# Optimization experiments

Measured on AMD Instinct MI355X. Metric: run time of the kernel, lower is better.

The kernel has to match this reference:

```python
import jax, jax.numpy as jnp
import numpy as np

B, T, M, D = 8, 512, 16, 128
P, H = 256, 8
E = P // H


def setup_inputs() -> dict:
    key = jax.random.key(0)
    ks = jax.random.split(key, 5)
    inp = jax.random.normal(ks[0], (B, T, M, D), dtype=jnp.float32)
    mask = jax.random.randint(ks[1], (B, T, M), 0, 2).astype(bool)
    sc = 1.0 / np.sqrt(D).astype(np.float32)
    Wq = jax.random.normal(ks[2], (D, P), dtype=jnp.float32) * sc
    Wk = jax.random.normal(ks[3], (D, P), dtype=jnp.float32) * sc
    Wv = jax.random.normal(ks[4], (D, P), dtype=jnp.float32) * sc
    z = jnp.zeros((P,), dtype=jnp.float32)
    return {"inp": inp, "mask": mask, "Wq": Wq, "bq": z, "Wk": Wk, "bk": z, "Wv": Wv, "bv": z}


def _split_heads(x):
    # (b, t, m, h*e) -> (b, m, h, t, e)
    b, t, m, _ = x.shape
    return x.reshape(b, t, m, H, E).transpose(0, 2, 3, 1, 4)


def reference(inp, mask, Wq, bq, Wk, bk, Wv, bv):
    q = _split_heads(inp @ Wq + bq)
    k = _split_heads(inp @ Wk + bk)
    v = _split_heads(inp @ Wv + bv)
    # scores over time axis per (batch, modality, head): (b, m, h, t, t)
    score = jnp.einsum('bmhte,bmhse->bmhts', q, k) / np.float32(np.sqrt(E))
    kmask = mask.transpose(0, 2, 1)[:, :, None, None, :]  # (b, m, 1, 1, t)
    score = jnp.where(kmask, score, -jnp.inf)
    weight = jax.nn.softmax(score, axis=-1)
    weight = jnp.where(kmask, weight, jnp.zeros((), weight.dtype))
    out = jnp.einsum('bmhts,bmhse->bmhte', weight, v)
    b, m, h, t, e = out.shape
    return out.transpose(0, 3, 1, 2, 4).reshape(b, t, m, h * e)
```

## Files before the change

### kernel.cpp

```cpp
#include <hip/hip_runtime.h>
#include <stdint.h>

#define B_ 8
#define T_ 512
#define M_ 16
#define D_ 128
#define P_ 256
#define H_ 8
#define E_ 32

typedef __attribute__((ext_vector_type(8))) short  short8;
typedef __attribute__((ext_vector_type(4))) short  short4v;
typedef __attribute__((ext_vector_type(4))) float  float4v;
typedef __attribute__((ext_vector_type(2))) unsigned int uint2v;
typedef __attribute__((ext_vector_type(4))) unsigned int uint4v;
typedef __attribute__((ext_vector_type(2))) __bf16 bf16x2;

#define MFMA32(a,b,c) __builtin_amdgcn_mfma_f32_16x16x32_bf16(a,b,c,0,0,0)
#define EXP2F(x) __builtin_amdgcn_exp2f(x)

#define C2 0.2550332772062413f

static __device__ __forceinline__ unsigned short f2bf(float x){
  unsigned int u = __builtin_bit_cast(unsigned int, x);
  u += 0x7FFFu + ((u >> 16) & 1u);
  return (unsigned short)(u >> 16);
}

static __device__ __forceinline__ unsigned int pk2(float a, float b){
  bf16x2 h; h[0] = (__bf16)a; h[1] = (__bf16)b;
  return __builtin_bit_cast(unsigned int, h);
}

static __device__ __forceinline__ short4v pack4(float4v v){
  uint2v u; u.x = pk2(v[0], v[1]); u.y = pk2(v[2], v[3]);
  return __builtin_bit_cast(short4v, u);
}

static __device__ __forceinline__ short8 pack8(float4v a, float4v b){
  uint4v u; u.x = pk2(a[0],a[1]); u.y = pk2(a[2],a[3]);
  u.z = pk2(b[0],b[1]); u.w = pk2(b[2],b[3]);
  return __builtin_bit_cast(short8, u);
}

static __device__ __forceinline__ short8 cat44(short4v lo, short4v hi){
  short8 r;
  r[0]=lo[0]; r[1]=lo[1]; r[2]=lo[2]; r[3]=lo[3];
  r[4]=hi[0]; r[5]=hi[1]; r[6]=hi[2]; r[7]=hi[3];
  return r;
}

__global__ void prep(const float* __restrict__ Wq, const float* __restrict__ Wk,
                     const float* __restrict__ Wv, uint16_t* __restrict__ WT){
  int idx = blockIdx.x*256 + threadIdx.x;
  int p = idx & (P_-1);
  int d = (idx >> 8) & (D_-1);
  int z = idx >> 15;
  int col = p;
  if (z < 2){
    int w = p & 31;
    int e = ((w>>2)&3)*8 + ((w>>4)&1)*4 + (w&3);
    col = (p & ~31) | e;
  }
  const float* W = (z==0) ? Wq : (z==1) ? Wk : Wv;
  float sc = (z==0) ? C2 : 1.0f;
  WT[(z<<15) + (p<<7) + d] = f2bf(W[d*P_ + col] * sc);
}

__global__ __launch_bounds__(512, 4) void attn_fused(
    const float* __restrict__ inp, const uint16_t* __restrict__ WT,
    const float* __restrict__ bq, const float* __restrict__ bk,
    const float* __restrict__ bv, const int* __restrict__ mask,
    float* __restrict__ out){
  __shared__ __align__(16) uint16_t smem[(65536 + 2048)/2];
  uint16_t* Kb   = smem;
  uint16_t* Vt   = smem + 16384;
  float*    Mrow = (float*)(smem + 32768);

  const int bx = blockIdx.x;
  const int h = bx >> 7, bm = bx & 127;
  const int b = bm >> 4, m = bm & 15;
  const int tid = threadIdx.x;
  const int wave = tid >> 6, lane = tid & 63;
  const int q4 = lane >> 4, c = lane & 15;
  const int t0 = wave*64;

  {
    int mv = mask[((size_t)(b*T_ + tid))*M_ + m];
    Mrow[tid] = mv ? 0.0f : -1e30f;
  }

  short8 af[4][4];
  {
    const float* src0 = inp + (size_t)((b*T_ + t0)*M_ + m)*D_ + c*4;
    for (int hh=0; hh<2; hh++){
      for (int jb=0; jb<2; jb++){
        float4v stg[8];
        for (int j=0; j<8; j++){
          int r = jb*32 + j*4 + q4;
          stg[j] = *(const float4v*)(src0 + (size_t)r*(M_*D_) + hh*64);
        }
        for (int j=0; j<8; j++){
          int r = t0 + jb*32 + j*4 + q4;
          short4v s4 = pack4(stg[j]);
          *(short4v*)(smem + r*64 + ((((c>>1) ^ (r&7))<<3) + ((c&1)<<2))) = s4;
        }
      }
      for (int tj=0; tj<4; tj++){
        int r2 = t0 + tj*16 + c;
        af[tj][hh*2+0] = *(const short8*)(smem + r2*64 + (((q4    ) ^ (r2&7))<<3));
        af[tj][hh*2+1] = *(const short8*)(smem + r2*64 + (((q4 | 4) ^ (r2&7))<<3));
      }
    }
  }
  __syncthreads();

  const uint16_t* WQ = WT                       + (size_t)(h*E_)*D_;
  const uint16_t* WK = WT + (size_t)1*P_*D_     + (size_t)(h*E_)*D_;
  const uint16_t* WV = WT + (size_t)2*P_*D_     + (size_t)(h*E_)*D_;
  float4v zf = {0.f,0.f,0.f,0.f};

  for (int eh=0; eh<2; eh++){
    float4v ka[4]; for (int j=0;j<4;j++) ka[j]=zf;
    for (int kc=0; kc<4; kc++){
      short8 w = *(const short8*)(WK + (size_t)(eh*16 + c)*D_ + kc*32 + q4*8);
      for (int sj=0; sj<4; sj++) ka[sj] = MFMA32(w, af[sj][kc], ka[sj]);
    }
    float4v bk4 = *(const float4v*)(bk + h*E_ + q4*8 + eh*4);
    for (int sj=0; sj<4; sj++){
      int s = t0 + sj*16 + c;
      short4v kv = pack4(ka[sj] + bk4);
      *(short4v*)(Kb + s*32 + ((q4 ^ (s&3))<<3) + eh*4) = kv;
    }
  }
  for (int eh=0; eh<2; eh++){
    float4v va[4]; for (int j=0;j<4;j++) va[j]=zf;
    for (int kc=0; kc<4; kc++){
      short8 w = *(const short8*)(WV + (size_t)(eh*16 + c)*D_ + kc*32 + q4*8);
      for (int sj=0; sj<4; sj++) va[sj] = MFMA32(w, af[sj][kc], va[sj]);
    }
    float4v bv4 = *(const float4v*)(bv + h*E_ + eh*16 + q4*4);
    for (int sj=0; sj<4; sj++){
      int s = t0 + sj*16 + c;
      short4v vv = pack4(va[sj] + bv4);
      for (int r=0; r<4; r++){
        int e = eh*16 + q4*4 + r;
        Vt[e*T_ + ((((s>>2) + 2*e) & 127)*4) + (s&3)] = (uint16_t)vv[r];
      }
    }
  }
  short8 q8[4];
  {
    short4v qtmp[4][2];
    for (int eh=0; eh<2; eh++){
      float4v qa[4]; for (int j=0;j<4;j++) qa[j]=zf;
      for (int kc=0; kc<4; kc++){
        short8 w = *(const short8*)(WQ + (size_t)(eh*16 + c)*D_ + kc*32 + q4*8);
        for (int tj=0; tj<4; tj++) qa[tj] = MFMA32(w, af[tj][kc], qa[tj]);
      }
      float4v bq4 = *(const float4v*)(bq + h*E_ + q4*8 + eh*4);
      bq4 *= C2;
      for (int tj=0; tj<4; tj++) qtmp[tj][eh] = pack4(qa[tj] + bq4);
    }
    for (int tj=0; tj<4; tj++) q8[tj] = cat44(qtmp[tj][0], qtmp[tj][1]);
  }
  __syncthreads();

  float4v O[4][2], L4[4];
  for (int i=0;i<4;i++){ O[i][0]=zf; O[i][1]=zf; L4[i]=zf; }
  const short one_bf = (short)0x3F80;
  short8 ones8;
  for (int i=0;i<8;i++) ones8[i] = one_bf;

  for (int sb=0; sb<16; sb++){
    const int sq = sb*32;
    float4v mm0 = *(const float4v*)(Mrow + sq + q4*4);
    float4v mm1 = *(const float4v*)(Mrow + sq + 16 + q4*4);
    const int srow0 = sq + c, srow1 = sq + 16 + c;
    short8 kb8_0 = *(const short8*)(Kb + srow0*32 + ((q4 ^ (srow0&3))<<3));
    short8 kb8_1 = *(const short8*)(Kb + srow1*32 + ((q4 ^ (srow1&3))<<3));
    const int u0 = sb*8 + q4, u1 = u0 + 4;
    short4v vA0 = *(const short4v*)(Vt + (size_t)c*T_      + ((u0 + 2*c     ) & 127)*4);
    short4v vA1 = *(const short4v*)(Vt + (size_t)c*T_      + ((u1 + 2*c     ) & 127)*4);
    short4v vB0 = *(const short4v*)(Vt + (size_t)(16+c)*T_ + ((u0 + 32 + 2*c) & 127)*4);
    short4v vB1 = *(const short4v*)(Vt + (size_t)(16+c)*T_ + ((u1 + 32 + 2*c) & 127)*4);
    short8 V8_0 = cat44(vA0, vA1);
    short8 V8_1 = cat44(vB0, vB1);
    __builtin_amdgcn_s_setprio(1);
    for (int tj=0; tj<4; tj++){
      float4v st0 = MFMA32(kb8_0, q8[tj], mm0);
      float4v st1 = MFMA32(kb8_1, q8[tj], mm1);
      float4v p0, p1;
      p0[0] = EXP2F(st0[0]); p0[1] = EXP2F(st0[1]);
      p0[2] = EXP2F(st0[2]); p0[3] = EXP2F(st0[3]);
      p1[0] = EXP2F(st1[0]); p1[1] = EXP2F(st1[1]);
      p1[2] = EXP2F(st1[2]); p1[3] = EXP2F(st1[3]);
      short8 A8 = pack8(p0, p1);
      O[tj][0] = MFMA32(A8, V8_0, O[tj][0]);
      O[tj][1] = MFMA32(A8, V8_1, O[tj][1]);
      L4[tj]   = MFMA32(A8, ones8, L4[tj]);
    }
    __builtin_amdgcn_s_setprio(0);
  }

  for (int ti=0; ti<4; ti++){
    float4v linv;
    for (int r=0; r<4; r++) linv[r] = __builtin_amdgcn_rcpf(L4[ti][r]);
    for (int ej=0; ej<2; ej++){
      float4v v = O[ti][ej] * linv;
      for (int r=0; r<4; r++){
        int t = t0 + ti*16 + q4*4 + r;
        out[(size_t)((b*T_ + t)*M_ + m)*P_ + h*E_ + ej*16 + c] = v[r];
      }
    }
  }
}

extern "C" void kernel_launch(void* const* d_in, const int* in_sizes, int n_in,
                              void* d_out, int out_size, void* d_ws, size_t ws_size,
                              hipStream_t stream){
  const float* inp = (const float*)d_in[0];
  const int*   msk = (const int*)  d_in[1];
  const float* Wq  = (const float*)d_in[2];
  const float* bq  = (const float*)d_in[3];
  const float* Wk  = (const float*)d_in[4];
  const float* bk  = (const float*)d_in[5];
  const float* Wv  = (const float*)d_in[6];
  const float* bv  = (const float*)d_in[7];
  float* out = (float*)d_out;

  uint16_t* WT = (uint16_t*)d_ws;

  prep<<<dim3(384), dim3(256), 0, stream>>>(Wq, Wk, Wv, WT);
  attn_fused<<<dim3(1024), dim3(512), 0, stream>>>(inp, WT, bq, bk, bv, msk, out);
}
```

Baseline: 164.3 us.

## Compact unmasked keys in shared memory and skip masked key blocks

Uses a ballot and prefix count to give each unmasked key position a compacted index. K and V for the head are written only at those indices, and the tail up to the next 32-row block is zero-filled. The attention loop then runs over only ceil(nv/32) key blocks instead of all 16. With a random mask about half the keys are valid, so roughly half of the QK/exp/PV work is removed, at the cost of an extra reduction step, scattered LDS writes and padding work.

```diff
diff --git a/kernel.cpp b/kernel.cpp
--- a/kernel.cpp
+++ b/kernel.cpp
@@ -72,10 +72,11 @@
     const float* __restrict__ bq, const float* __restrict__ bk,
     const float* __restrict__ bv, const int* __restrict__ mask,
     float* __restrict__ out){
-  __shared__ __align__(16) uint16_t smem[(65536 + 2048)/2];
+  __shared__ __align__(16) uint16_t smem[(65536 + 2048 + 64)/2];
   uint16_t* Kb   = smem;
   uint16_t* Vt   = smem + 16384;
-  float*    Mrow = (float*)(smem + 32768);
+  float*    Madd = (float*)(smem + 32768);
+  int*      wcnt = (int*)(smem + 32768 + 1024);
 
   const int bx = blockIdx.x;
   const int h = bx >> 7, bm = bx & 127;
@@ -85,10 +86,7 @@
   const int q4 = lane >> 4, c = lane & 15;
   const int t0 = wave*64;
 
-  {
-    int mv = mask[((size_t)(b*T_ + tid))*M_ + m];
-    Mrow[tid] = mv ? 0.0f : -1e30f;
-  }
+  const int mv = mask[((size_t)(b*T_ + tid))*M_ + m];
 
   short8 af[4][4];
   {
@@ -113,7 +111,34 @@
       }
     }
   }
+
+  const unsigned long long bal = __ballot(mv != 0);
+  const int lanepfx = __popcll(bal & ((1ull << lane) - 1ull));
+  if (lane == 0) wcnt[wave] = __popcll(bal);
+
   __syncthreads();
+
+  int off = 0, nv = 0;
+  for (int w = 0; w < 8; w++){
+    int cw = wcnt[w];
+    nv += cw;
+    if (w < wave) off += cw;
+  }
+  nv = __builtin_amdgcn_readfirstlane(nv);
+  const int nsb = (nv + 31) >> 5;
+  const int myt = (mv != 0) ? (off + lanepfx) : -1;
+
+  Madd[tid] = (tid < nv) ? 0.0f : -1e30f;
+  for (int j = nv + tid; j < nsb*32; j += 512){
+    short8 z8 = {0,0,0,0,0,0,0,0};
+    short8* kp = (short8*)(Kb + j*32);
+    kp[0]=z8; kp[1]=z8; kp[2]=z8; kp[3]=z8;
+    for (int e = 0; e < E_; e++)
+      Vt[e*T_ + ((((j>>2) + 2*e) & 127)*4) + (j&3)] = 0;
+  }
+
+  int tg[4];
+  for (int sj = 0; sj < 4; sj++) tg[sj] = __shfl(myt, sj*16 + c);
 
   const uint16_t* WQ = WT                       + (size_t)(h*E_)*D_;
   const uint16_t* WK = WT + (size_t)1*P_*D_     + (size_t)(h*E_)*D_;
@@ -128,9 +153,10 @@
     }
     float4v bk4 = *(const float4v*)(bk + h*E_ + q4*8 + eh*4);
     for (int sj=0; sj<4; sj++){
-      int s = t0 + sj*16 + c;
+      int t = tg[sj];
       short4v kv = pack4(ka[sj] + bk4);
-      *(short4v*)(Kb + s*32 + ((q4 ^ (s&3))<<3) + eh*4) = kv;
+      if (t >= 0)
+        *(short4v*)(Kb + t*32 + ((q4 ^ (t&3))<<3) + eh*4) = kv;
     }
   }
   for (int eh=0; eh<2; eh++){
@@ -141,11 +167,13 @@
     }
     float4v bv4 = *(const float4v*)(bv + h*E_ + eh*16 + q4*4);
     for (int sj=0; sj<4; sj++){
-      int s = t0 + sj*16 + c;
+      int t = tg[sj];
       short4v vv = pack4(va[sj] + bv4);
-      for (int r=0; r<4; r++){
-        int e = eh*16 + q4*4 + r;
-        Vt[e*T_ + ((((s>>2) + 2*e) & 127)*4) + (s&3)] = (uint16_t)vv[r];
+      if (t >= 0){
+        for (int r=0; r<4; r++){
+          int e = eh*16 + q4*4 + r;
+          Vt[e*T_ + ((((t>>2) + 2*e) & 127)*4) + (t&3)] = (uint16_t)vv[r];
+        }
       }
     }
   }
@@ -172,10 +200,10 @@
   short8 ones8;
   for (int i=0;i<8;i++) ones8[i] = one_bf;
 
-  for (int sb=0; sb<16; sb++){
+  for (int sb=0; sb<nsb; sb++){
     const int sq = sb*32;
-    float4v mm0 = *(const float4v*)(Mrow + sq + q4*4);
-    float4v mm1 = *(const float4v*)(Mrow + sq + 16 + q4*4);
+    float4v mm0 = *(const float4v*)(Madd + sq + q4*4);
+    float4v mm1 = *(const float4v*)(Madd + sq + 16 + q4*4);
     const int srow0 = sq + c, srow1 = sq + 16 + c;
     short8 kb8_0 = *(const short8*)(Kb + srow0*32 + ((q4 ^ (srow0&3))<<3));
     short8 kb8_1 = *(const short8*)(Kb + srow1*32 + ((q4 ^ (srow1&3))<<3));
```

New measurement: 155.2 us. 5.6% less time.
